# Optimization experiments

Measured on AMD Instinct MI355X. Metric: run time of the kernel, lower is better.

Reference implementation:

```python
import jax, jax.numpy as jnp
import numpy as np

D_MODEL = 1024
N_HEADS = 16
THETA = 10000.0


def _rope(x, token_positions):
    # x: (b, h, s, d_k); token_positions: (b, s)
    d_k = x.shape[-1]
    powers = jnp.arange(0, d_k, 2, dtype=jnp.float32) / d_k        # (d_k/2,)
    freqs = 1.0 / (THETA ** powers)
    ang = token_positions.astype(jnp.float32)[..., None] * freqs   # (b, s, d_k/2)
    cos = jnp.cos(ang)[:, None, :, :].astype(x.dtype)              # (b, 1, s, d_k/2)
    sin = jnp.sin(ang)[:, None, :, :].astype(x.dtype)
    x_even = x[..., ::2]
    x_odd = x[..., 1::2]
    r1 = x_even * cos - x_odd * sin
    r2 = x_even * sin + x_odd * cos
    # interleave back to (..., d_k)
    return jnp.stack([r1, r2], axis=-1).reshape(x.shape)


def reference(x, token_positions, wq, wk, wv, wo):
    B, S, D = x.shape
    H = N_HEADS
    d_k = D // H

    def proj(w):
        y = jnp.einsum('bsi,oi->bso', x, w)
        return y.reshape(B, S, H, d_k).transpose(0, 2, 1, 3)  # (b, h, s, d_k)

    q = _rope(proj(wq), token_positions)
    k = _rope(proj(wk), token_positions)
    v = proj(wv)

    scale = 1.0 / jnp.sqrt(jnp.asarray(d_k, dtype=x.dtype))
    score = jnp.einsum('bhqd,bhkd->bhqk', q, k) * scale  # (b, h, s, s)
    causal = jnp.tril(jnp.ones((S, S), dtype=bool))
    score = jnp.where(causal, score, -jnp.inf)
    probs = jax.nn.softmax(score, axis=-1)
    attn = jnp.einsum('bhqk,bhkd->bhqd', probs, v)
    attn = attn.transpose(0, 2, 1, 3).reshape(B, S, D)
    return jnp.einsum('bsi,oi->bso', attn, wo)


def setup_inputs() -> dict:
    key = jax.random.key(0)
    ks = jax.random.split(key, 6)
    B, S, D = 2, 2048, D_MODEL
    std = (2.0 / (D + D)) ** 0.5
    x = jax.random.normal(ks[0], (B, S, D), dtype=jnp.float32)
    token_positions = jnp.broadcast_to(jnp.arange(S, dtype=jnp.int32), (B, S))
    wq = jax.random.normal(ks[1], (D, D), dtype=jnp.float32) * std
    wk = jax.random.normal(ks[2], (D, D), dtype=jnp.float32) * std
    wv = jax.random.normal(ks[3], (D, D), dtype=jnp.float32) * std
    wo = jax.random.normal(ks[4], (D, D), dtype=jnp.float32) * std
    return {"x": x, "token_positions": token_positions, "wq": wq, "wk": wk, "wv": wv, "wo": wo}
```

## Files before the change

kernel.cpp:

```cpp
#include <hip/hip_runtime.h>
#include <hip/hip_bf16.h>

typedef unsigned short u16;
typedef unsigned int u32;
typedef short short8 __attribute__((ext_vector_type(8)));
typedef u16 u16x8 __attribute__((ext_vector_type(8)));
typedef u16 u16x4 __attribute__((ext_vector_type(4)));
typedef u32 u32x4 __attribute__((ext_vector_type(4)));
typedef float f32x4 __attribute__((ext_vector_type(4)));
typedef float f32x16 __attribute__((ext_vector_type(16)));

#define MFMA(a, b, c) __builtin_amdgcn_mfma_f32_16x16x32_bf16((a), (b), (c), 0, 0, 0)
#define MFMA32(a, b, c) __builtin_amdgcn_mfma_f32_32x32x16_bf16((a), (b), (c), 0, 0, 0)

#define QSCALE 0.18033688011112042f

__device__ __forceinline__ u16 f2bf(float f) {
  unsigned u = __float_as_uint(f);
  unsigned r = (u + 0x7fffu + ((u >> 16) & 1u)) >> 16;
  return (u16)r;
}
__device__ __forceinline__ float bf2f(u16 h) {
  return __uint_as_float(((unsigned)h) << 16);
}
__device__ __forceinline__ float exp2hw(float x) {
  float r;
  asm("v_exp_f32 %0, %1" : "=v"(r) : "v"(x));
  return r;
}
__device__ __forceinline__ u32 cvtpk(float lo, float hi) {
  u32 d;
  asm("v_cvt_pk_bf16_f32 %0, %1, %2" : "=v"(d) : "v"(lo), "v"(hi));
  return d;
}
__device__ __forceinline__ void plswap(u32& a, u32& b) {
  asm volatile("v_permlane32_swap_b32 %0, %1" : "+v"(a), "+v"(b));
}
__device__ __forceinline__ void async16(const void* g, void* l) {
  __builtin_amdgcn_global_load_lds(
      (const __attribute__((address_space(1))) void*)g,
      (__attribute__((address_space(3))) void*)l, 16, 0, 0);
}
__device__ __forceinline__ f32x16 zero16() {
  f32x16 z;
#pragma unroll
  for (int i = 0; i < 16; i++) z[i] = 0.f;
  return z;
}
#define WAITV(N) asm volatile("s_waitcnt vmcnt(" #N ")" ::: "memory")
#define WAITL0() asm volatile("s_waitcnt lgkmcnt(0)" ::: "memory")
#define BAR() __builtin_amdgcn_s_barrier()
#define PRIO1 __builtin_amdgcn_s_setprio(1)
#define PRIO0 __builtin_amdgcn_s_setprio(0)

__global__ __launch_bounds__(256) void convert_kernel(
    const float* __restrict__ x, const float* __restrict__ wq,
    const float* __restrict__ wk, const float* __restrict__ wv,
    const float* __restrict__ wo, u16* __restrict__ ws) {
  int blk = blockIdx.x;
  const float* src; u16* dst;
  if (blk < 2048)      { src = x;  dst = ws; }
  else if (blk < 2560) { src = wq; dst = ws + 4194304;               blk -= 2048; }
  else if (blk < 3072) { src = wk; dst = ws + 4194304 + 1048576;     blk -= 2560; }
  else if (blk < 3584) { src = wv; dst = ws + 4194304 + 2 * 1048576; blk -= 3072; }
  else                 { src = wo; dst = ws + 4194304 + 3 * 1048576; blk -= 3584; }
  int idx = (blk * 256 + threadIdx.x) * 8;
  float4 v0 = *(const float4*)(src + idx);
  float4 v1 = *(const float4*)(src + idx + 4);
  u16x8 o;
  o[0] = f2bf(v0.x); o[1] = f2bf(v0.y); o[2] = f2bf(v0.z); o[3] = f2bf(v0.w);
  o[4] = f2bf(v1.x); o[5] = f2bf(v1.y); o[6] = f2bf(v1.z); o[7] = f2bf(v1.w);
  *(u16x8*)(dst + idx) = o;
}

__global__ __launch_bounds__(256) void rope_table(const int* __restrict__ tp,
                                                  float* __restrict__ tab) {
  int t = blockIdx.x * 256 + threadIdx.x;
  int bs = t >> 5, p = t & 31;
  float freq = exp2hw(-(float)p * 0.4152410118609203f);
  float ang = (float)tp[bs] * freq;
  float sn, cs;
  sincosf(ang, &sn, &cs);
  tab[bs * 64 + p * 2] = cs;
  tab[bs * 64 + p * 2 + 1] = sn;
}

__global__ __launch_bounds__(512, 2) void gemm_qkv256(
    const u16* __restrict__ xb, const u16* __restrict__ wqb,
    const u16* __restrict__ wkb, const u16* __restrict__ wvb,
    const float* __restrict__ tab, u16* __restrict__ qb, u16* __restrict__ kb,
    u16* __restrict__ vt) {
  __shared__ u16 As[2][2][8192];
  __shared__ u16 Bs[2][2][8192];
  const int tid = threadIdx.x, lane = tid & 63, wid = tid >> 6;
  const int wm = wid >> 2, wn = wid & 3;
  const int g = lane >> 4, r = lane & 15;
  const int z = blockIdx.z;
  const u16* Ag = xb;
  const u16* Bg = (z == 0) ? wqb : (z == 1) ? wkb : wvb;
  const int rowBase = blockIdx.y << 8, colBase = blockIdx.x << 8;

  const int c0 = tid, c1 = tid + 512;
  const int sr0 = c0 >> 3, sk0 = ((c0 & 7) ^ (sr0 & 7)) * 8;
  const int sr1 = c1 >> 3, sk1 = ((c1 & 7) ^ (sr1 & 7)) * 8;

#define STG_A(BUF, H, T)                                                      \
  do {                                                                        \
    async16(Ag + (size_t)(rowBase + (H)*128 + sr0) * 1024 + (T)*64 + sk0,     \
            (char*)As[BUF][H] + c0 * 16);                                     \
    async16(Ag + (size_t)(rowBase + (H)*128 + sr1) * 1024 + (T)*64 + sk1,     \
            (char*)As[BUF][H] + c1 * 16);                                     \
  } while (0)
#define STG_B(BUF, H, T)                                                      \
  do {                                                                        \
    async16(Bg + (size_t)(colBase + (H)*128 + sr0) * 1024 + (T)*64 + sk0,     \
            (char*)Bs[BUF][H] + c0 * 16);                                     \
    async16(Bg + (size_t)(colBase + (H)*128 + sr1) * 1024 + (T)*64 + sk1,     \
            (char*)Bs[BUF][H] + c1 * 16);                                     \
  } while (0)

  f32x4 acc[8][4];
#pragma unroll
  for (int m = 0; m < 8; m++)
#pragma unroll
    for (int n = 0; n < 4; n++) acc[m][n] = (f32x4){0.f, 0.f, 0.f, 0.f};
  short8 af[4][2], bfr[4][2];

#define RD_A(CUR, MH)                                                         \
  do {                                                                        \
    _Pragma("unroll") for (int mi = 0; mi < 4; mi++) {                        \
      int ra = (MH)*64 + mi * 16 + r;                                         \
      const u16* p = As[CUR][wm] + ra * 64;                                   \
      int sw = (ra & 7) << 3;                                                 \
      af[mi][0] = *(const short8*)(p + ((g << 3) ^ sw));                      \
      af[mi][1] = *(const short8*)(p + (((4 + g) << 3) ^ sw));                \
    }                                                                         \
  } while (0)
#define RD_B(CUR, NP)                                                         \
  do {                                                                        \
    _Pragma("unroll") for (int ni = 0; ni < 2; ni++) {                        \
      int cb = wn * 64 + ((NP)*2 + ni) * 16 + r;                              \
      const u16* p = Bs[CUR][cb >> 7] + (cb & 127) * 64;                      \
      int sw = (cb & 7) << 3;                                                 \
      bfr[(NP)*2 + ni][0] = *(const short8*)(p + ((g << 3) ^ sw));            \
      bfr[(NP)*2 + ni][1] = *(const short8*)(p + (((4 + g) << 3) ^ sw));      \
    }                                                                         \
  } while (0)
#define MM16(MH, NP)                                                          \
  do {                                                                        \
    _Pragma("unroll") for (int mi = 0; mi < 4; mi++)                          \
        _Pragma("unroll") for (int ni = 0; ni < 2; ni++) {                    \
      acc[(MH)*4 + mi][(NP)*2 + ni] = MFMA(af[mi][0], bfr[(NP)*2 + ni][0],    \
                                           acc[(MH)*4 + mi][(NP)*2 + ni]);    \
      acc[(MH)*4 + mi][(NP)*2 + ni] = MFMA(af[mi][1], bfr[(NP)*2 + ni][1],    \
                                           acc[(MH)*4 + mi][(NP)*2 + ni]);    \
    }                                                                         \
  } while (0)

  STG_A(0, 0, 0); STG_A(0, 1, 0); STG_B(0, 0, 0); STG_B(0, 1, 0);
  STG_A(1, 0, 1); STG_A(1, 1, 1);
  WAITV(4);
  BAR();

  for (int t = 0; t < 16; ++t) {
    const int cur = t & 1, nxt = cur ^ 1;
    RD_A(cur, 0);
    RD_B(cur, 0); RD_B(cur, 1);
    if (t < 15) { STG_B(nxt, 0, t + 1); STG_B(nxt, 1, t + 1); }
    BAR(); WAITL0();
    PRIO1; MM16(0, 0); MM16(0, 1); PRIO0; BAR();
    RD_A(cur, 1);
    if (t < 14) {
      STG_A(cur, 0, t + 2); STG_A(cur, 1, t + 2);
      WAITV(4);
    } else {
      WAITV(0);
    }
    BAR(); WAITL0();
    PRIO1; MM16(1, 0); MM16(1, 1); PRIO0; BAR();
  }
#undef STG_A
#undef STG_B
#undef RD_A
#undef RD_B
#undef MM16

  if (z < 2) {
    u16* dst = z ? kb : qb;
    const float qs = z ? 1.0f : QSCALE;
#pragma unroll
    for (int m = 0; m < 8; m++)
#pragma unroll
      for (int n = 0; n < 4; n++) {
        const int col = colBase + wn * 64 + n * 16 + r;
        const int p2 = (col >> 1) & 31;
        const bool odd = col & 1;
#pragma unroll
        for (int i = 0; i < 4; i++) {
          const int row = rowBase + wm * 128 + m * 16 + g * 4 + i;
          float2 cssn = *(const float2*)(tab + row * 64 + p2 * 2);
          float v = acc[m][n][i];
          float part = __shfl_xor(v, 1);
          float res = odd ? (part * cssn.y + v * cssn.x)
                          : (v * cssn.x - part * cssn.y);
          dst[(size_t)row * 1024 + col] = f2bf(res * qs);
        }
      }
  } else {
#pragma unroll
    for (int m = 0; m < 8; m++)
#pragma unroll
      for (int n = 0; n < 4; n++)
#pragma unroll
        for (int i = 0; i < 4; i++) {
          int row = rowBase + wm * 128 + m * 16 + g * 4 + i;
          int col = colBase + wn * 64 + n * 16 + r;
          int b = row >> 11, s = row & 2047;
          vt[(size_t)((b * 16 + (col >> 6)) * 64 + (col & 63)) * 2048 + s] =
              f2bf(acc[m][n][i]);
        }
  }
}

__device__ __forceinline__ void gemm_tile(const u16* __restrict__ A,
                                          const u16* __restrict__ Bm, int K,
                                          int rowBase, int colBase, u16* As,
                                          u16* Bs, f32x4 acc[4][4]) {
  const int tid = threadIdx.x;
  const int lane = tid & 63, wid = tid >> 6;
  const int wr = wid >> 1, wc = wid & 1;
  const int g = lane >> 4, r = lane & 15;

#pragma unroll
  for (int m = 0; m < 4; m++)
#pragma unroll
    for (int n = 0; n < 4; n++) acc[m][n] = (f32x4){0.f, 0.f, 0.f, 0.f};

#define GSTAGE(KT, BUF)                                                       \
  do {                                                                        \
    _Pragma("unroll") for (int i_ = 0; i_ < 4; ++i_) {                        \
      int c = i_ * 256 + tid;                                                 \
      int row = c >> 3, kc = (c & 7) ^ (row & 7);                             \
      async16(A + (size_t)(rowBase + row) * K + ((KT) << 6) + kc * 8,         \
              (char*)As + (BUF)*16384 + c * 16);                              \
    }                                                                         \
    _Pragma("unroll") for (int i_ = 0; i_ < 4; ++i_) {                        \
      int c = i_ * 256 + tid;                                                 \
      int row = c >> 3, kc = (c & 7) ^ (row & 7);                             \
      async16(Bm + (size_t)(colBase + row) * K + ((KT) << 6) + kc * 8,        \
              (char*)Bs + (BUF)*16384 + c * 16);                              \
    }                                                                         \
  } while (0)

  const int nkt = K >> 6;
  GSTAGE(0, 0);
  for (int kt = 0; kt < nkt; ++kt) {
    const int cur = kt & 1;
    if (kt + 1 < nkt) {
      GSTAGE(kt + 1, cur ^ 1);
      WAITV(8);
    } else {
      WAITV(0);
    }
    BAR();
    const u16* Ab = As + cur * 8192;
    const u16* Bb = Bs + cur * 8192;
#pragma unroll
    for (int ks = 0; ks < 2; ++ks) {
      short8 af[4], bfr[4];
#pragma unroll
      for (int m = 0; m < 4; m++) {
        int rr = wr * 64 + m * 16 + r;
        af[m] = *(const short8*)(Ab + rr * 64 + (((ks * 4 + g) ^ (rr & 7)) << 3));
      }
#pragma unroll
      for (int n = 0; n < 4; n++) {
        int rr = wc * 64 + n * 16 + r;
        bfr[n] = *(const short8*)(Bb + rr * 64 + (((ks * 4 + g) ^ (rr & 7)) << 3));
      }
#pragma unroll
      for (int m = 0; m < 4; m++)
#pragma unroll
        for (int n = 0; n < 4; n++)
          acc[m][n] = MFMA(af[m], bfr[n], acc[m][n]);
    }
    WAITL0();
    BAR();
  }
#undef GSTAGE
}

__global__ __launch_bounds__(256, 4) void attn_kernel(
    const u16* __restrict__ qg, const u16* __restrict__ kg,
    const u16* __restrict__ vt, u16* __restrict__ p0, u16* __restrict__ p1,
    float* __restrict__ mbuf, float* __restrict__ lbuf) {
  __shared__ u16 Ks[2][64 * 64];
  __shared__ u16 Vs[2][64 * 64];
  const int tid = threadIdx.x, wid = tid >> 6, lane = tid & 63;
  const int q5 = lane & 31, hi = lane >> 5;
  const int akc = blockIdx.x >> 5, bh = blockIdx.x & 31;
  const int a = akc >> 2, k = (akc >> 1) & 1, c = akc & 1;
  const int b = bh >> 4, h = bh & 15;
  const int base = (wid < 2) ? a : (15 - a);
  const int rb = base * 128 + k * 64 + (wid & 1) * 32;
  const int cmax = rb >> 5;
  const int jend = 30 - 2 * a + k;
  const int qrow = (b << 11) + rb + q5;

  short8 bq[4];
  {
    const u16* qp = qg + (size_t)qrow * 1024 + (h << 6) + hi * 8;
    bq[0] = *(const short8*)(qp);
    bq[1] = *(const short8*)(qp + 16);
    bq[2] = *(const short8*)(qp + 32);
    bq[3] = *(const short8*)(qp + 48);
  }
  f32x16 accO0 = zero16(), accO1 = zero16();
  float m_r = -1e30f, l_r = 0.f;

#define STAGE(JT, BUF)                                                        \
  do {                                                                        \
    _Pragma("unroll") for (int i_ = 0; i_ < 2; i_++) {                        \
      int cc_ = i_ * 256 + tid;                                               \
      int row = cc_ >> 3, cc = (cc_ & 7) ^ (row & 7);                         \
      async16(kg + (size_t)((b << 11) + ((JT) << 6) + row) * 1024 +           \
                  (h << 6) + cc * 8,                                          \
              (char*)Ks[BUF] + cc_ * 16);                                     \
      async16(vt + (size_t)((bh << 6) + row) * 2048 + ((JT) << 6) + cc * 8,   \
              (char*)Vs[BUF] + cc_ * 16);                                     \
    }                                                                         \
  } while (0)

  if (c <= jend) STAGE(c, 0);

  for (int jj = c; jj <= jend; jj += 2) {
    const int cur = ((jj - c) >> 1) & 1;
    if (jj + 2 <= jend) {
      STAGE(jj + 2, cur ^ 1);
      WAITV(4);
    } else {
      WAITV(0);
    }
    BAR();
    if (2 * jj <= cmax) {
      const u16* Kb = Ks[cur];
      const u16* Vb = Vs[cur];
      const bool has1 = (2 * jj + 1 <= cmax);
      const int rsw = (q5 & 7) << 3;
      f32x16 s0 = zero16(), s1 = zero16();
      PRIO1;
#pragma unroll
      for (int kk = 0; kk < 4; kk++) {
        short8 kf =
            *(const short8*)(Kb + q5 * 64 + ((((kk << 1) + hi) << 3) ^ rsw));
        s0 = MFMA32(kf, bq[kk], s0);
      }
      PRIO0;
      if (has1) {
        PRIO1;
#pragma unroll
        for (int kk = 0; kk < 4; kk++) {
          short8 kf = *(const short8*)(Kb + (32 + q5) * 64 +
                                       ((((kk << 1) + hi) << 3) ^ rsw));
          s1 = MFMA32(kf, bq[kk], s1);
        }
        PRIO0;
      }
      if (2 * jj == cmax) {
#pragma unroll
        for (int rg = 0; rg < 16; rg++) {
          int rowk = (rg & 3) + 8 * (rg >> 2) + 4 * hi;
          if (rowk > q5) s0[rg] = -1e30f;
        }
      } else if (2 * jj + 1 == cmax) {
#pragma unroll
        for (int rg = 0; rg < 16; rg++) {
          int rowk = (rg & 3) + 8 * (rg >> 2) + 4 * hi;
          if (rowk > q5) s1[rg] = -1e30f;
        }
      }
      float pmax = s0[0];
#pragma unroll
      for (int rg = 1; rg < 16; rg++) pmax = fmaxf(pmax, s0[rg]);
      if (has1) {
#pragma unroll
        for (int rg = 0; rg < 16; rg++) pmax = fmaxf(pmax, s1[rg]);
      }
      pmax = fmaxf(pmax, __shfl_xor(pmax, 32));
      if (!__all(pmax <= m_r + 8.0f)) {
        float mn = fmaxf(m_r, pmax);
        float sc = exp2hw(m_r - mn);
        l_r *= sc;
#pragma unroll
        for (int rg = 0; rg < 16; rg++) {
          accO0[rg] *= sc;
          accO1[rg] *= sc;
        }
        m_r = mn;
      }
      float rs = 0.f;
      u32 pw00[4], pw01[4], pw10[4], pw11[4];
#define PACK(SREG, OUT, S16)                                                  \
  do {                                                                        \
    float pp0 = exp2hw(SREG[(S16)*8 + 0] - m_r);                              \
    float pp1 = exp2hw(SREG[(S16)*8 + 1] - m_r);                              \
    float pp2 = exp2hw(SREG[(S16)*8 + 2] - m_r);                              \
    float pp3 = exp2hw(SREG[(S16)*8 + 3] - m_r);                              \
    float pp4 = exp2hw(SREG[(S16)*8 + 4] - m_r);                              \
    float pp5 = exp2hw(SREG[(S16)*8 + 5] - m_r);                              \
    float pp6 = exp2hw(SREG[(S16)*8 + 6] - m_r);                              \
    float pp7 = exp2hw(SREG[(S16)*8 + 7] - m_r);                              \
    rs += ((pp0 + pp1) + (pp2 + pp3)) + ((pp4 + pp5) + (pp6 + pp7));          \
    u32 X = cvtpk(pp0, pp1), Y = cvtpk(pp2, pp3);                             \
    u32 U = cvtpk(pp4, pp5), W = cvtpk(pp6, pp7);                             \
    plswap(X, U);                                                             \
    plswap(Y, W);                                                             \
    OUT[0] = X; OUT[1] = Y; OUT[2] = U; OUT[3] = W;                           \
  } while (0)
      PACK(s0, pw00, 0);
      PACK(s0, pw01, 1);
      if (has1) {
        PACK(s1, pw10, 0);
        PACK(s1, pw11, 1);
      }
#undef PACK
      rs += __shfl_xor(rs, 32);
      l_r += rs;
#define PVSTEP(PW, CH)                                                        \
  do {                                                                        \
    u32x4 pv_ = {PW[0], PW[1], PW[2], PW[3]};                                 \
    short8 pb_ = __builtin_bit_cast(short8, pv_);                             \
    short8 v0_ =                                                              \
        *(const short8*)(Vb + q5 * 64 + ((((CH) + hi) << 3) ^ rsw));          \
    short8 v1_ = *(const short8*)(Vb + (32 + q5) * 64 +                       \
                                  ((((CH) + hi) << 3) ^ rsw));                \
    accO0 = MFMA32(v0_, pb_, accO0);                                          \
    accO1 = MFMA32(v1_, pb_, accO1);                                          \
  } while (0)
      PRIO1;
      PVSTEP(pw00, 0);
      PVSTEP(pw01, 2);
      if (has1) {
        PVSTEP(pw10, 4);
        PVSTEP(pw11, 6);
      }
      PRIO0;
#undef PVSTEP
    }
    WAITL0();
    BAR();
  }
#undef STAGE

  u16* pout = c ? p1 : p0;
#pragma unroll
  for (int qd = 0; qd < 4; qd++) {
    u16x4 o0, o1;
#pragma unroll
    for (int e = 0; e < 4; e++) {
      o0[e] = f2bf(accO0[qd * 4 + e]);
      o1[e] = f2bf(accO1[qd * 4 + e]);
    }
    u16* op = pout + (size_t)qrow * 1024 + (h << 6) + qd * 8 + hi * 4;
    *(u16x4*)(op) = o0;
    *(u16x4*)(op + 32) = o1;
  }
  if (hi == 0) {
    int mli = c * 65536 + (bh << 11) + rb + q5;
    mbuf[mli] = m_r;
    lbuf[mli] = l_r;
  }
}

__global__ __launch_bounds__(256) void attn_merge(const u16* __restrict__ p1,
                                                  const float* __restrict__ mbuf,
                                                  const float* __restrict__ lbuf,
                                                  u16* __restrict__ ab) {
  int t = blockIdx.x * 256 + threadIdx.x;
  int dg = t & 7, row = t >> 3;
  int bh = row >> 11, s = row & 2047;
  int b = bh >> 4, h = bh & 15;
  size_t addr = (size_t)((b << 11) + s) * 1024 + (h << 6) + dg * 8;
  float m0 = mbuf[row], m1 = mbuf[65536 + row];
  float l0 = lbuf[row], l1 = lbuf[65536 + row];
  float m = fmaxf(m0, m1);
  float w0 = exp2hw(m0 - m), w1 = exp2hw(m1 - m);
  float inv = 1.0f / (l0 * w0 + l1 * w1);
  u16x8 o0 = *(const u16x8*)(ab + addr);
  u16x8 o1 = *(const u16x8*)(p1 + addr);
  u16x8 o;
#pragma unroll
  for (int i = 0; i < 8; i++)
    o[i] = f2bf((bf2f(o0[i]) * w0 + bf2f(o1[i]) * w1) * inv);
  *(u16x8*)(ab + addr) = o;
}

__global__ __launch_bounds__(256) void gemm_ao(const u16* __restrict__ ab,
                                               const u16* __restrict__ wob,
                                               float* __restrict__ out) {
  __shared__ u16 As[2][128 * 64], Bs[2][128 * 64];
  f32x4 acc[4][4];
  gemm_tile(ab, wob, 1024, blockIdx.y * 128, blockIdx.x * 128, As[0], Bs[0], acc);
  const int lane = threadIdx.x & 63, wid = threadIdx.x >> 6;
  const int wr = wid >> 1, wc = wid & 1, g = lane >> 4, r = lane & 15;
  const int rowB = blockIdx.y * 128 + wr * 64;
  const int colB = blockIdx.x * 128 + wc * 64;
#pragma unroll
  for (int m = 0; m < 4; m++)
#pragma unroll
    for (int n = 0; n < 4; n++)
#pragma unroll
      for (int i = 0; i < 4; i++)
        out[(size_t)(rowB + m * 16 + g * 4 + i) * 1024 + colB + n * 16 + r] =
            acc[m][n][i];
}

extern "C" void kernel_launch(void* const* d_in, const int* in_sizes, int n_in,
                              void* d_out, int out_size, void* d_ws,
                              size_t ws_size, hipStream_t stream) {
  const float* x = (const float*)d_in[0];
  const int* tp = (const int*)d_in[1];
  const float* wq = (const float*)d_in[2];
  const float* wk = (const float*)d_in[3];
  const float* wv = (const float*)d_in[4];
  const float* wo = (const float*)d_in[5];
  float* out = (float*)d_out;

  u16* ws = (u16*)d_ws;
  u16* xb = ws;
  u16* wqb = xb + 4194304;
  u16* wkb = wqb + 1048576;
  u16* wvb = wkb + 1048576;
  u16* wob = wvb + 1048576;
  u16* qb = wob + 1048576;
  u16* kb = qb + 4194304;
  u16* vtb = kb + 4194304;
  u16* ab = vtb + 4194304;
  float* tab = (float*)ab;
  float* mbuf = (float*)wqb;
  float* lbuf = (float*)wkb;

  convert_kernel<<<4096, 256, 0, stream>>>(x, wq, wk, wv, wo, ws);
  rope_table<<<512, 256, 0, stream>>>(tp, tab);
  gemm_qkv256<<<dim3(4, 16, 3), 512, 0, stream>>>(xb, wqb, wkb, wvb, tab, qb,
                                                  kb, vtb);
  attn_kernel<<<1024, 256, 0, stream>>>(qb, kb, vtb, ab, xb, mbuf, lbuf);
  attn_merge<<<2048, 256, 0, stream>>>(xb, mbuf, lbuf, ab);
  gemm_ao<<<dim3(8, 32), 256, 0, stream>>>(ab, wob, out);
}
```

Baseline: 118.0 us.

## Retile fused QKV GEMM to 256x192 tiles over concatenated weight

The QKV projection now treats wq, wk and wv as one contiguous 3072-row weight matrix and uses 256x192 output tiles. This gives a 16x16 grid of 256 blocks instead of 4x16x3 = 192, so the workload maps more evenly onto the 256 CUs. The epilogue picks Q, K or V per 16-column slice from the global column index. The cost is a narrower B tile, so each A tile is reused across fewer columns, and the code assumes the converted weights sit back to back in the workspace.

```diff
diff --git a/kernel.cpp b/kernel.cpp
--- a/kernel.cpp
+++ b/kernel.cpp
@@ -86,115 +86,113 @@
 }
 
 __global__ __launch_bounds__(512, 2) void gemm_qkv256(
-    const u16* __restrict__ xb, const u16* __restrict__ wqb,
-    const u16* __restrict__ wkb, const u16* __restrict__ wvb,
+    const u16* __restrict__ xb, const u16* __restrict__ Wg,
     const float* __restrict__ tab, u16* __restrict__ qb, u16* __restrict__ kb,
     u16* __restrict__ vt) {
-  __shared__ u16 As[2][2][8192];
-  __shared__ u16 Bs[2][2][8192];
+  __shared__ u16 As[2][16384];
+  __shared__ u16 Bs[2][12288];
   const int tid = threadIdx.x, lane = tid & 63, wid = tid >> 6;
   const int wm = wid >> 2, wn = wid & 3;
   const int g = lane >> 4, r = lane & 15;
-  const int z = blockIdx.z;
-  const u16* Ag = xb;
-  const u16* Bg = (z == 0) ? wqb : (z == 1) ? wkb : wvb;
-  const int rowBase = blockIdx.y << 8, colBase = blockIdx.x << 8;
-
-  const int c0 = tid, c1 = tid + 512;
-  const int sr0 = c0 >> 3, sk0 = ((c0 & 7) ^ (sr0 & 7)) * 8;
-  const int sr1 = c1 >> 3, sk1 = ((c1 & 7) ^ (sr1 & 7)) * 8;
-
-#define STG_A(BUF, H, T)                                                      \
-  do {                                                                        \
-    async16(Ag + (size_t)(rowBase + (H)*128 + sr0) * 1024 + (T)*64 + sk0,     \
-            (char*)As[BUF][H] + c0 * 16);                                     \
-    async16(Ag + (size_t)(rowBase + (H)*128 + sr1) * 1024 + (T)*64 + sk1,     \
-            (char*)As[BUF][H] + c1 * 16);                                     \
-  } while (0)
-#define STG_B(BUF, H, T)                                                      \
-  do {                                                                        \
-    async16(Bg + (size_t)(colBase + (H)*128 + sr0) * 1024 + (T)*64 + sk0,     \
-            (char*)Bs[BUF][H] + c0 * 16);                                     \
-    async16(Bg + (size_t)(colBase + (H)*128 + sr1) * 1024 + (T)*64 + sk1,     \
-            (char*)Bs[BUF][H] + c1 * 16);                                     \
-  } while (0)
-
-  f32x4 acc[8][4];
+  const int rowBase = blockIdx.y << 8;
+  const int colBase = blockIdx.x * 192;
+
+#define STG_A(BUF, T)                                                         \
+  do {                                                                        \
+    _Pragma("unroll") for (int i_ = 0; i_ < 4; ++i_) {                        \
+      int c = i_ * 512 + tid;                                                 \
+      int row = c >> 3, kc = ((c & 7) ^ (row & 7)) * 8;                       \
+      async16(xb + (size_t)(rowBase + row) * 1024 + (T)*64 + kc,              \
+              (char*)As[BUF] + c * 16);                                       \
+    }                                                                         \
+  } while (0)
+#define STG_B(BUF, T)                                                         \
+  do {                                                                        \
+    _Pragma("unroll") for (int i_ = 0; i_ < 3; ++i_) {                        \
+      int c = i_ * 512 + tid;                                                 \
+      int row = c >> 3, kc = ((c & 7) ^ (row & 7)) * 8;                       \
+      async16(Wg + (size_t)(colBase + row) * 1024 + (T)*64 + kc,              \
+              (char*)Bs[BUF] + c * 16);                                       \
+    }                                                                         \
+  } while (0)
+
+  f32x4 acc[8][3];
 #pragma unroll
   for (int m = 0; m < 8; m++)
 #pragma unroll
-    for (int n = 0; n < 4; n++) acc[m][n] = (f32x4){0.f, 0.f, 0.f, 0.f};
-  short8 af[4][2], bfr[4][2];
+    for (int n = 0; n < 3; n++) acc[m][n] = (f32x4){0.f, 0.f, 0.f, 0.f};
+  short8 af[4][2], bfr[3][2];
 
 #define RD_A(CUR, MH)                                                         \
   do {                                                                        \
     _Pragma("unroll") for (int mi = 0; mi < 4; mi++) {                        \
-      int ra = (MH)*64 + mi * 16 + r;                                         \
-      const u16* p = As[CUR][wm] + ra * 64;                                   \
+      int ra = wm * 128 + (MH)*64 + mi * 16 + r;                              \
+      const u16* p = As[CUR] + ra * 64;                                       \
       int sw = (ra & 7) << 3;                                                 \
       af[mi][0] = *(const short8*)(p + ((g << 3) ^ sw));                      \
       af[mi][1] = *(const short8*)(p + (((4 + g) << 3) ^ sw));                \
     }                                                                         \
   } while (0)
-#define RD_B(CUR, NP)                                                         \
-  do {                                                                        \
-    _Pragma("unroll") for (int ni = 0; ni < 2; ni++) {                        \
-      int cb = wn * 64 + ((NP)*2 + ni) * 16 + r;                              \
-      const u16* p = Bs[CUR][cb >> 7] + (cb & 127) * 64;                      \
+#define RD_B(CUR)                                                             \
+  do {                                                                        \
+    _Pragma("unroll") for (int ni = 0; ni < 3; ni++) {                        \
+      int cb = wn * 48 + ni * 16 + r;                                         \
+      const u16* p = Bs[CUR] + cb * 64;                                       \
       int sw = (cb & 7) << 3;                                                 \
-      bfr[(NP)*2 + ni][0] = *(const short8*)(p + ((g << 3) ^ sw));            \
-      bfr[(NP)*2 + ni][1] = *(const short8*)(p + (((4 + g) << 3) ^ sw));      \
-    }                                                                         \
-  } while (0)
-#define MM16(MH, NP)                                                          \
+      bfr[ni][0] = *(const short8*)(p + ((g << 3) ^ sw));                     \
+      bfr[ni][1] = *(const short8*)(p + (((4 + g) << 3) ^ sw));               \
+    }                                                                         \
+  } while (0)
+#define MM24(MH)                                                              \
   do {                                                                        \
     _Pragma("unroll") for (int mi = 0; mi < 4; mi++)                          \
-        _Pragma("unroll") for (int ni = 0; ni < 2; ni++) {                    \
-      acc[(MH)*4 + mi][(NP)*2 + ni] = MFMA(af[mi][0], bfr[(NP)*2 + ni][0],    \
-                                           acc[(MH)*4 + mi][(NP)*2 + ni]);    \
-      acc[(MH)*4 + mi][(NP)*2 + ni] = MFMA(af[mi][1], bfr[(NP)*2 + ni][1],    \
-                                           acc[(MH)*4 + mi][(NP)*2 + ni]);    \
-    }                                                                         \
-  } while (0)
-
-  STG_A(0, 0, 0); STG_A(0, 1, 0); STG_B(0, 0, 0); STG_B(0, 1, 0);
-  STG_A(1, 0, 1); STG_A(1, 1, 1);
+        _Pragma("unroll") for (int ni = 0; ni < 3; ni++) {                    \
+      acc[(MH)*4 + mi][ni] = MFMA(af[mi][0], bfr[ni][0], acc[(MH)*4 + mi][ni]); \
+      acc[(MH)*4 + mi][ni] = MFMA(af[mi][1], bfr[ni][1], acc[(MH)*4 + mi][ni]); \
+    }                                                                         \
+  } while (0)
+
+  STG_A(0, 0); STG_B(0, 0);
+  STG_A(1, 1);
   WAITV(4);
   BAR();
 
   for (int t = 0; t < 16; ++t) {
     const int cur = t & 1, nxt = cur ^ 1;
     RD_A(cur, 0);
-    RD_B(cur, 0); RD_B(cur, 1);
-    if (t < 15) { STG_B(nxt, 0, t + 1); STG_B(nxt, 1, t + 1); }
+    RD_B(cur);
+    if (t < 15) STG_B(nxt, t + 1);
     BAR(); WAITL0();
-    PRIO1; MM16(0, 0); MM16(0, 1); PRIO0; BAR();
+    PRIO1; MM24(0); PRIO0; BAR();
     RD_A(cur, 1);
     if (t < 14) {
-      STG_A(cur, 0, t + 2); STG_A(cur, 1, t + 2);
+      STG_A(cur, t + 2);
       WAITV(4);
     } else {
       WAITV(0);
     }
     BAR(); WAITL0();
-    PRIO1; MM16(1, 0); MM16(1, 1); PRIO0; BAR();
+    PRIO1; MM24(1); PRIO0; BAR();
   }
 #undef STG_A
 #undef STG_B
 #undef RD_A
 #undef RD_B
-#undef MM16
-
-  if (z < 2) {
-    u16* dst = z ? kb : qb;
-    const float qs = z ? 1.0f : QSCALE;
-#pragma unroll
-    for (int m = 0; m < 8; m++)
-#pragma unroll
-      for (int n = 0; n < 4; n++) {
-        const int col = colBase + wn * 64 + n * 16 + r;
-        const int p2 = (col >> 1) & 31;
-        const bool odd = col & 1;
+#undef MM24
+
+  const int colF = colBase + wn * 48;
+#pragma unroll
+  for (int n = 0; n < 3; n++) {
+    const int col3 = colF + n * 16 + r;
+    const int z = col3 >> 10;
+    const int col = col3 & 1023;
+    if (z < 2) {
+      u16* dst = z ? kb : qb;
+      const float qs = z ? 1.0f : QSCALE;
+      const int p2 = (col >> 1) & 31;
+      const bool odd = col & 1;
+#pragma unroll
+      for (int m = 0; m < 8; m++)
 #pragma unroll
         for (int i = 0; i < 4; i++) {
           const int row = rowBase + wm * 128 + m * 16 + g * 4 + i;
@@ -205,20 +203,17 @@
                           : (v * cssn.x - part * cssn.y);
           dst[(size_t)row * 1024 + col] = f2bf(res * qs);
         }
-      }
-  } else {
-#pragma unroll
-    for (int m = 0; m < 8; m++)
-#pragma unroll
-      for (int n = 0; n < 4; n++)
+    } else {
+#pragma unroll
+      for (int m = 0; m < 8; m++)
 #pragma unroll
         for (int i = 0; i < 4; i++) {
-          int row = rowBase + wm * 128 + m * 16 + g * 4 + i;
-          int col = colBase + wn * 64 + n * 16 + r;
-          int b = row >> 11, s = row & 2047;
-          vt[(size_t)((b * 16 + (col >> 6)) * 64 + (col & 63)) * 2048 + s] =
+          const int row = rowBase + wm * 128 + m * 16 + g * 4 + i;
+          const int bb = row >> 11, s = row & 2047;
+          vt[(size_t)((bb * 16 + (col >> 6)) * 64 + (col & 63)) * 2048 + s] =
               f2bf(acc[m][n][i]);
         }
+    }
   }
 }
 
@@ -542,8 +537,7 @@
 
   convert_kernel<<<4096, 256, 0, stream>>>(x, wq, wk, wv, wo, ws);
   rope_table<<<512, 256, 0, stream>>>(tp, tab);
-  gemm_qkv256<<<dim3(4, 16, 3), 512, 0, stream>>>(xb, wqb, wkb, wvb, tab, qb,
-                                                  kb, vtb);
+  gemm_qkv256<<<dim3(16, 16), 512, 0, stream>>>(xb, wqb, tab, qb, kb, vtb);
   attn_kernel<<<1024, 256, 0, stream>>>(qb, kb, vtb, ab, xb, mbuf, lbuf);
   attn_merge<<<2048, 256, 0, stream>>>(xb, mbuf, lbuf, ab);
   gemm_ao<<<dim3(8, 32), 256, 0, stream>>>(ab, wob, out);
```

After: 115.5 us. -2.1%, faster.
